# Optimization experiments

Hardware: AMD Instinct MI355X
Metric: run time of the kernel (lower is better)

Reference implementation:

```python
import jax, jax.numpy as jnp
import numpy as np

B, S, D = 4, 2048, 512
H, HD = 8, 64            # n_heads, head_dim = D // H
E, K, F = 8, 2, 1024     # n_experts, top_k, d_ff
EPS = 1e-6


def setup_inputs() -> dict:
    key = jax.random.key(0)
    ks = jax.random.split(key, 16)
    sd = 0.02
    return {
        "inputs": jax.random.normal(ks[0], (B, S, D), jnp.float32),
        "rms1_w": jnp.ones((D,), jnp.float32),
        "wq": jax.random.normal(ks[1], (D, H, HD), jnp.float32) * sd,
        "bq": jnp.zeros((H, HD), jnp.float32),
        "wk": jax.random.normal(ks[2], (D, H, HD), jnp.float32) * sd,
        "bk": jnp.zeros((H, HD), jnp.float32),
        "wv": jax.random.normal(ks[3], (D, H, HD), jnp.float32) * sd,
        "bv": jnp.zeros((H, HD), jnp.float32),
        "wo": jax.random.normal(ks[4], (H, HD, D), jnp.float32) * sd,
        "bo": jnp.zeros((D,), jnp.float32),
        "rms2_w": jnp.ones((D,), jnp.float32),
        "gate_w": jax.random.normal(ks[5], (D, E), jnp.float32) * sd,
        "ew1": jax.random.normal(ks[6], (E, D, F), jnp.float32) * sd,
        "eb1": jnp.zeros((E, F), jnp.float32),
        "ew2": jax.random.normal(ks[7], (E, F, D), jnp.float32) * sd,
        "eb2": jnp.zeros((E, D), jnp.float32),
    }


def _rmsnorm(x, w):
    return x * jax.lax.rsqrt(jnp.mean(x * x, axis=-1, keepdims=True) + EPS) * w


def _mha(x, wq, bq, wk, bk, wv, bv, wo, bo):
    q = jnp.einsum("bsd,dhe->bshe", x, wq) + bq
    k = jnp.einsum("bsd,dhe->bshe", x, wk) + bk
    v = jnp.einsum("bsd,dhe->bshe", x, wv) + bv
    scores = jnp.einsum("bqhe,bkhe->bhqk", q, k) / jnp.sqrt(jnp.float32(HD))
    attn = jax.nn.softmax(scores, axis=-1)
    ctx = jnp.einsum("bhqk,bkhe->bqhe", attn, v)
    return jnp.einsum("bqhe,hed->bqd", ctx, wo) + bo


def _moe(x, gate_w, ew1, eb1, ew2, eb2):
    T = B * S
    xt = x.reshape(T, D)
    probs = jax.nn.softmax(xt @ gate_w, axis=-1)          # [T, E]
    topv, topi = jax.lax.top_k(probs, K)                   # [T, K]
    topv = topv / jnp.sum(topv, axis=-1, keepdims=True)    # renormalize
    # dense combine weights [T, E]
    wmat = jnp.sum(jax.nn.one_hot(topi, E, dtype=xt.dtype) * topv[..., None], axis=1)
    h = jax.nn.relu(jnp.einsum("td,edf->tef", xt, ew1) + eb1)   # [T, E, F]
    y = jnp.einsum("tef,efd->ted", h, ew2) + eb2                # [T, E, D]
    out = jnp.einsum("te,ted->td", wmat, y)
    return out.reshape(B, S, D)


def reference(inputs, rms1_w, wq, bq, wk, bk, wv, bv, wo, bo, rms2_w, gate_w, ew1, eb1, ew2, eb2):
    x = _rmsnorm(inputs, rms1_w)
    x = _mha(x, wq, bq, wk, bk, wv, bv, wo, bo)
    x1 = x + inputs
    x = _rmsnorm(x1, rms2_w)
    x = _moe(x, gate_w, ew1, eb1, ew2, eb2)
    # dropout is identity at inference
    return x + x1
```

## Files before the change

kernel.cpp:

```cpp
#include <hip/hip_runtime.h>
#include <hip/hip_bf16.h>

typedef unsigned short u16;
typedef __attribute__((ext_vector_type(8))) short short8;
typedef __attribute__((ext_vector_type(4))) short bf16x4;
typedef __attribute__((ext_vector_type(4))) float f32x4;
typedef __attribute__((ext_vector_type(4))) int i32x4;
typedef __attribute__((ext_vector_type(2))) unsigned u32x2;

#define DEV __device__ __forceinline__

DEV float bf2f(u16 v){ unsigned u = ((unsigned)v)<<16; float f; __builtin_memcpy(&f,&u,4); return f; }
DEV u16 f2bf(float f){ unsigned u; __builtin_memcpy(&u,&f,4); u += 0x7fff + ((u>>16)&1); return (u16)(u>>16); }

DEV void gload16(const void* g, void* l){
  __builtin_amdgcn_global_load_lds((const __attribute__((address_space(1))) void*)g,
                                   (__attribute__((address_space(3))) void*)l, 16, 0, 0);
}

DEV unsigned packbf2(float a, float b){
  float2 f = {a, b};
  __hip_bfloat162 h = __float22bfloat162_rn(f);
  unsigned w; __builtin_memcpy(&w, &h, 4);
  return w;
}


__global__ __launch_bounds__(256) void k_tconv4(const float* __restrict__ s0, const float* __restrict__ s1,
    const float* __restrict__ s2, const float* __restrict__ s3, u16* __restrict__ dst){
  int z = blockIdx.z;
  const float* src = z==0 ? s0 : (z==1 ? s1 : (z==2 ? s2 : s3));
  dst += (size_t)z * 512 * 512;
  int r0 = blockIdx.y * 64, c0 = blockIdx.x * 64;
  __shared__ u16 tile[64][68];
  int tid = threadIdx.x;
  int rr = tid >> 4, cc = (tid & 15) * 4;
  #pragma unroll
  for (int it = 0; it < 4; ++it){
    int r = it*16 + rr;
    float4 v = *(const float4*)(src + (size_t)(r0 + r)*512 + c0 + cc);
    bf16x4 pk = { (short)f2bf(v.x), (short)f2bf(v.y), (short)f2bf(v.z), (short)f2bf(v.w) };
    *(bf16x4*)&tile[r][cc] = pk;
  }
  __syncthreads();
  #pragma unroll
  for (int it = 0; it < 4; ++it){
    int c = it*16 + rr;
    bf16x4 pk = { (short)tile[cc+0][c], (short)tile[cc+1][c],
                  (short)tile[cc+2][c], (short)tile[cc+3][c] };
    *(bf16x4*)(dst + (size_t)(c0 + c)*512 + r0 + cc) = pk;
  }
}

__global__ __launch_bounds__(256) void k_tconv(const float* __restrict__ src, u16* __restrict__ dst,
    int R, int C){
  src += (size_t)blockIdx.z * R * C;
  dst += (size_t)blockIdx.z * R * C;
  int r0 = blockIdx.y * 64, c0 = blockIdx.x * 64;
  __shared__ u16 tile[64][68];
  int tid = threadIdx.x;
  int rr = tid >> 4, cc = (tid & 15) * 4;
  #pragma unroll
  for (int it = 0; it < 4; ++it){
    int r = it*16 + rr;
    float4 v = *(const float4*)(src + (size_t)(r0 + r)*C + c0 + cc);
    bf16x4 pk = { (short)f2bf(v.x), (short)f2bf(v.y), (short)f2bf(v.z), (short)f2bf(v.w) };
    *(bf16x4*)&tile[r][cc] = pk;
  }
  __syncthreads();
  #pragma unroll
  for (int it = 0; it < 4; ++it){
    int c = it*16 + rr;
    bf16x4 pk = { (short)tile[cc+0][c], (short)tile[cc+1][c],
                  (short)tile[cc+2][c], (short)tile[cc+3][c] };
    *(bf16x4*)(dst + (size_t)(c0 + c)*R + r0 + cc) = pk;
  }
}

__global__ __launch_bounds__(256) void k_vtrans(const u16* __restrict__ src, u16* __restrict__ dst){
  int bh = blockIdx.y; int s0 = blockIdx.x*64;
  src += (size_t)bh*2048*64 + (size_t)s0*64;
  dst += (size_t)bh*64*2048 + s0;
  __shared__ unsigned tile[64*33];
  int tid = threadIdx.x;
  #pragma unroll
  for (int it = 0; it < 2; ++it){
    int c = tid + it*256;
    int r = c >> 3, c8 = c & 7;
    i32x4 v = *(const i32x4*)(src + (size_t)r*64 + c8*8);
    *(i32x4*)&tile[r*33 + c8*4] = v;
  }
  __syncthreads();
  #pragma unroll
  for (int it = 0; it < 2; ++it){
    int c = tid + it*256;
    int d = c >> 3, s8 = c & 7;
    union { i32x4 v; u16 us[8]; } o;
    #pragma unroll
    for (int j = 0; j < 8; ++j){
      unsigned w = tile[(s8*8+j)*33 + (d>>1)];
      o.us[j] = (d & 1) ? (u16)(w >> 16) : (u16)(w & 0xffff);
    }
    *(i32x4*)(dst + (size_t)d*2048 + s8*8) = o.v;
  }
}

__global__ __launch_bounds__(256) void k_rmsnorm(const float* __restrict__ x, const float* __restrict__ w,
    u16* __restrict__ ob){
  int t = blockIdx.x, tid = threadIdx.x;
  const float* xr = x + (size_t)t*512;
  float2 v = *(const float2*)(xr + tid*2);
  float ss = v.x*v.x + v.y*v.y;
  #pragma unroll
  for (int o=32; o>0; o>>=1) ss += __shfl_down(ss, o);
  __shared__ float sred[4];
  if ((tid&63)==0) sred[tid>>6] = ss;
  __syncthreads();
  float tot = sred[0]+sred[1]+sred[2]+sred[3];
  float inv = rsqrtf(tot*(1.f/512.f) + 1e-6f);
  float2 wv = *(const float2*)(w + tid*2);
  ob[(size_t)t*512 + tid*2]     = f2bf(v.x*inv*wv.x);
  ob[(size_t)t*512 + tid*2 + 1] = f2bf(v.y*inv*wv.y);
}

__global__ __launch_bounds__(256) void k_rmsgate(const float* __restrict__ x, const float* __restrict__ w,
    const float* __restrict__ gw, u16* __restrict__ ob, int* __restrict__ topi, float* __restrict__ topw){
  int t = blockIdx.x, tid = threadIdx.x;
  const float* xr = x + (size_t)t*512;
  float2 v = *(const float2*)(xr + tid*2);
  float ss = v.x*v.x + v.y*v.y;
  #pragma unroll
  for (int o=32; o>0; o>>=1) ss += __shfl_down(ss, o);
  __shared__ float sred[4];
  if ((tid&63)==0) sred[tid>>6] = ss;
  __syncthreads();
  float tot = sred[0]+sred[1]+sred[2]+sred[3];
  float inv = rsqrtf(tot*(1.f/512.f) + 1e-6f);
  float2 wv = *(const float2*)(w + tid*2);
  float y0 = v.x*inv*wv.x, y1 = v.y*inv*wv.y;
  ob[(size_t)t*512 + tid*2]     = f2bf(y0);
  ob[(size_t)t*512 + tid*2 + 1] = f2bf(y1);
  float acc[8];
  const float* g0 = gw + tid*16;
  #pragma unroll
  for (int e=0;e<8;e++) acc[e] = y0*g0[e] + y1*g0[8+e];
  #pragma unroll
  for (int dd=1; dd<64; dd<<=1)
    #pragma unroll
    for (int e=0;e<8;e++) acc[e] += __shfl_xor(acc[e], dd);
  __shared__ float gred[4][8];
  if ((tid&63)==0)
    #pragma unroll
    for (int e=0;e<8;e++) gred[tid>>6][e] = acc[e];
  __syncthreads();
  if (tid==0){
    float l[8];
    #pragma unroll
    for (int e=0;e<8;e++) l[e] = gred[0][e]+gred[1][e]+gred[2][e]+gred[3][e];
    int i0=0; float a0=l[0];
    #pragma unroll
    for (int e=1;e<8;e++) if (l[e]>a0){ a0=l[e]; i0=e; }
    int i1=-1; float a1=-1e30f;
    #pragma unroll
    for (int e=0;e<8;e++) if (e!=i0 && l[e]>a1){ a1=l[e]; i1=e; }
    float w1 = __expf(a1 - a0);
    float invs = 1.f / (1.f + w1);
    topi[t*2]=i0; topi[t*2+1]=i1;
    topw[t*2]=invs; topw[t*2+1]=w1*invs;
  }
}

__global__ __launch_bounds__(256) void k_count(const int* __restrict__ topi, int* __restrict__ counts){
  __shared__ int lcnt[8];
  if (threadIdx.x < 8) lcnt[threadIdx.x] = 0;
  __syncthreads();
  for (int i = blockIdx.x*256 + threadIdx.x; i < 16384; i += 256*64)
    atomicAdd(&lcnt[topi[i]], 1);
  __syncthreads();
  if (threadIdx.x < 8) atomicAdd(&counts[threadIdx.x], lcnt[threadIdx.x]);
}

template<int MODE>
__global__ __launch_bounds__(256) void k_gemm(const u16* __restrict__ A, const u16* __restrict__ Bt,
    int Nsize, int Ksize,
    const float* __restrict__ b0, const float* __restrict__ b1, const float* __restrict__ b2,
    const float* __restrict__ resid, float* __restrict__ outf,
    u16* __restrict__ o0, u16* __restrict__ o1, u16* __restrict__ o2,
    const int* __restrict__ ebase, const int* __restrict__ ecnt, const int* __restrict__ etok)
{
  int nNT = Nsize >> 7;
  int e=0, mt, nt, myBase=0, myCnt=0;
  if constexpr (MODE>=2){
    e = blockIdx.x & 7;
    int rr = blockIdx.x >> 3;
    mt = rr / nNT; nt = rr - mt*nNT;
    myCnt = ecnt[e]; myBase = ebase[e];
    if (mt*128 >= myCnt) return;
    Bt += (size_t)e * Nsize * Ksize;
  } else {
    int q = gridDim.x >> 3;
    int bid = blockIdx.x;
    int swb = (bid & 7)*q + (bid >> 3);
    mt = swb / nNT; nt = swb - mt*nNT;
  }
  __shared__ u16 As[2][128*32];
  __shared__ u16 Bs[2][128*32];
  int tid = threadIdx.x;
  int lane = tid & 63, wid = tid >> 6;
  int wr = (wid>>1)<<6, wc = (wid&1)<<6;
  int lrow = lane & 15, lk8 = (lane>>4)<<3;
  const u16* asrc[2]; const u16* bsrc[2];
  int ldoff[2];
  #pragma unroll
  for (int it=0; it<2; ++it){
    int c = it*256 + tid;
    int r = c >> 2, c4 = c & 3;
    int grow;
    if constexpr (MODE==2){
      int ml = mt*128 + r; if (ml >= myCnt) ml = myCnt-1;
      grow = etok[myBase + ml];
    } else if constexpr (MODE==3){
      int ml = mt*128 + r; if (ml >= myCnt) ml = myCnt-1;
      grow = myBase + ml;
    } else {
      grow = mt*128 + r;
    }
    asrc[it] = A + (size_t)grow*Ksize + c4*8;
    bsrc[it] = Bt + (size_t)(nt*128 + r)*Ksize + c4*8;
    ldoff[it] = (it*256 + wid*64)*8;
  }
  f32x4 acc[4][4] = {};
  int nK = Ksize >> 5;
  #pragma unroll
  for (int it=0; it<2; ++it){
    gload16(asrc[it], &As[0][ldoff[it]]);
    gload16(bsrc[it], &Bs[0][ldoff[it]]);
  }
  __syncthreads();
  for (int ks = 0; ks < nK; ++ks){
    int cur = ks & 1;
    if (ks+1 < nK){
      int k0 = (ks+1) << 5;
      #pragma unroll
      for (int it=0; it<2; ++it){
        gload16(asrc[it] + k0, &As[cur^1][ldoff[it]]);
        gload16(bsrc[it] + k0, &Bs[cur^1][ldoff[it]]);
      }
    }
    short8 a[4], b[4];
    #pragma unroll
    for (int i=0;i<4;i++) a[i] = *(const short8*)(&As[cur][(wr + i*16 + lrow)*32 + lk8]);
    #pragma unroll
    for (int j=0;j<4;j++) b[j] = *(const short8*)(&Bs[cur][(wc + j*16 + lrow)*32 + lk8]);
    #pragma unroll
    for (int i=0;i<4;i++)
      #pragma unroll
      for (int j=0;j<4;j++)
        acc[i][j] = __builtin_amdgcn_mfma_f32_16x16x32_bf16(a[i], b[j], acc[i][j], 0,0,0);
    __syncthreads();
  }
  #pragma unroll
  for (int i=0;i<4;i++){
    #pragma unroll
    for (int r=0;r<4;r++){
      int rowl = mt*128 + wr + i*16 + ((lane>>4)<<2) + r;
      #pragma unroll
      for (int j=0;j<4;j++){
        int col = nt*128 + wc + j*16 + lrow;
        float v = acc[i][j][r];
        if constexpr (MODE==0){
          int which = col >> 9; int hc = col & 511;
          const float* bias = which==0 ? b0 : (which==1 ? b1 : b2);
          v += bias[hc];
          if (which == 0) v *= 0.18033688011112042f;
          u16* dst = which==0 ? o0 : (which==1 ? o1 : o2);
          int bidx = rowl >> 11, s = rowl & 2047;
          int h = hc >> 6, hd = hc & 63;
          dst[((size_t)(bidx*8+h)*2048 + s)*64 + hd] = f2bf(v);
        } else if constexpr (MODE==1){
          v += b0[col] + resid[(size_t)rowl*512 + col];
          outf[(size_t)rowl*512 + col] = v;
        } else if constexpr (MODE==2){
          if (rowl < myCnt){
            v += b0[e*1024 + col];
            v = fmaxf(v, 0.f);
            o0[(size_t)(myBase+rowl)*1024 + col] = f2bf(v);
          }
        } else {
          if (rowl < myCnt){
            v += b0[e*512 + col];
            o0[(size_t)(myBase+rowl)*512 + col] = f2bf(v);
          }
        }
      }
    }
  }
}

__global__ __launch_bounds__(512) void k_attn(const u16* __restrict__ qb, const u16* __restrict__ kb,
    const u16* __restrict__ vtb, u16* __restrict__ ctx)
{
  int bh = blockIdx.x & 31;
  int qt = blockIdx.x >> 5;
  int b = bh >> 3, h = bh & 7;
  const size_t bho = (size_t)bh * (2048*64);
  int tid = threadIdx.x, lane = tid & 63, wid = tid >> 6;
  int lrow = lane & 15, g = lane >> 4;
  __shared__ u16 Ks[128*64];
  __shared__ u16 Vts[64*128];
  __shared__ u16 Ps[8][16*128];
  char* Ksb = (char*)Ks;
  char* Vsb = (char*)Vts;
  char* Psb = (char*)&Ps[wid][0];
  int q0 = qt*128 + wid*16;
  short8 qf[2];
  #pragma unroll
  for (int kf=0;kf<2;kf++)
    qf[kf] = *(const short8*)(qb + bho + (size_t)(q0 + lrow)*64 + kf*32 + g*8);
  f32x4 oacc[4] = {};
  float lpart = 0.f;
  const int swz = (lrow & 7) << 4;

  size_t ksrc[2], vsrc[2];
  int kdst[2], vdst[2];
  #pragma unroll
  for (int it=0; it<2; ++it){
    int c = tid + it*512;
    int kr = c >> 3, kc8 = c & 7;
    ksrc[it] = bho + (size_t)kr*64 + kc8*8;
    kdst[it] = kr*128 + ((kc8*16) ^ ((kr&7)<<4));
    int vr = c >> 4, vc16 = c & 15;
    vsrc[it] = bho + (size_t)vr*2048 + vc16*8;
    vdst[it] = vr*256 + ((vc16*16) ^ ((vr&7)<<4));
  }
  i32x4 kreg[2], vreg[2];
  #pragma unroll
  for (int it=0; it<2; ++it){
    kreg[it] = *(const i32x4*)(kb + ksrc[it]);
    vreg[it] = *(const i32x4*)(vtb + vsrc[it]);
  }
  #pragma unroll
  for (int it=0; it<2; ++it){
    *(i32x4*)(Ksb + kdst[it]) = kreg[it];
    *(i32x4*)(Vsb + vdst[it]) = vreg[it];
  }
  __syncthreads();

  for (int kt=0; kt<16; ++kt){
    if (kt < 15){
      int k0 = (kt+1)*128;
      #pragma unroll
      for (int it=0; it<2; ++it){
        kreg[it] = *(const i32x4*)(kb + ksrc[it] + (size_t)k0*64);
        vreg[it] = *(const i32x4*)(vtb + vsrc[it] + k0);
      }
    }
    __builtin_amdgcn_s_setprio(1);
    #pragma unroll
    for (int nf=0; nf<8; ++nf){
      short8 kf0 = *(const short8*)(Ksb + (nf*16+lrow)*128 + ((g*16) ^ swz));
      short8 kf1 = *(const short8*)(Ksb + (nf*16+lrow)*128 + ((64 + g*16) ^ swz));
      f32x4 s = {};
      s = __builtin_amdgcn_mfma_f32_16x16x32_bf16(kf0, qf[0], s, 0,0,0);
      s = __builtin_amdgcn_mfma_f32_16x16x32_bf16(kf1, qf[1], s, 0,0,0);
      float p0 = __builtin_amdgcn_exp2f(s[0]);
      float p1 = __builtin_amdgcn_exp2f(s[1]);
      float p2 = __builtin_amdgcn_exp2f(s[2]);
      float p3 = __builtin_amdgcn_exp2f(s[3]);
      lpart += (p0+p1)+(p2+p3);
      *(u32x2*)(Psb + lrow*256 + ((nf*32 + g*8) ^ swz)) = (u32x2){packbf2(p0,p1), packbf2(p2,p3)};
    }
    short8 pfr[4];
    #pragma unroll
    for (int kf=0;kf<4;kf++)
      pfr[kf] = *(const short8*)(Psb + lrow*256 + ((kf*64 + g*16) ^ swz));
    #pragma unroll
    for (int dn=0;dn<4;dn++){
      #pragma unroll
      for (int kf=0;kf<4;kf++){
        short8 vf = *(const short8*)(Vsb + (dn*16+lrow)*256 + ((kf*64 + g*16) ^ swz));
        oacc[dn] = __builtin_amdgcn_mfma_f32_16x16x32_bf16(pfr[kf], vf, oacc[dn], 0,0,0);
      }
    }
    __builtin_amdgcn_s_setprio(0);
    __syncthreads();
    if (kt < 15){
      #pragma unroll
      for (int it=0; it<2; ++it){
        *(i32x4*)(Ksb + kdst[it]) = kreg[it];
        *(i32x4*)(Vsb + vdst[it]) = vreg[it];
      }
      __syncthreads();
    }
  }
  float ls = lpart;
  ls += __shfl_xor(ls, 16);
  ls += __shfl_xor(ls, 32);
  float linv[4];
  #pragma unroll
  for (int r=0;r<4;r++)
    linv[r] = 1.0f / __shfl(ls, g*4 + r);
  #pragma unroll
  for (int r=0;r<4;r++){
    int qrow = q0 + g*4 + r;
    #pragma unroll
    for (int dn=0;dn<4;dn++)
      ctx[((size_t)(b*2048 + qrow))*512 + h*64 + dn*16 + lrow] = f2bf(oacc[dn][r] * linv[r]);
  }
}

__global__ void k_scan(const int* __restrict__ counts, int* __restrict__ base, int* __restrict__ cur){
  if (threadIdx.x==0 && blockIdx.x==0){
    int s=0;
    for (int e=0;e<8;e++){ base[e]=s; cur[e]=s; s+=counts[e]; }
  }
}

__global__ __launch_bounds__(256) void k_assign(const int* __restrict__ topi,
    int* __restrict__ cur, int* __restrict__ rowof, int* __restrict__ tokof)
{
  __shared__ int lcnt[8];
  __shared__ int gbase[8];
  int tid = threadIdx.x;
  if (tid < 8) lcnt[tid] = 0;
  __syncthreads();
  int t = blockIdx.x*256 + tid;
  int e0 = topi[t*2], e1 = topi[t*2+1];
  int r0 = atomicAdd(&lcnt[e0], 1);
  int r1 = atomicAdd(&lcnt[e1], 1);
  __syncthreads();
  if (tid < 8) gbase[tid] = atomicAdd(&cur[tid], lcnt[tid]);
  __syncthreads();
  int row0 = gbase[e0] + r0, row1 = gbase[e1] + r1;
  rowof[t*2]   = row0;  rowof[t*2+1] = row1;
  tokof[row0] = t;      tokof[row1] = t;
}

__global__ __launch_bounds__(256) void k_combine(const float* __restrict__ x1, const u16* __restrict__ y,
    const int* __restrict__ rowof, const float* __restrict__ topw, float* __restrict__ out)
{
  int idx = blockIdx.x*256 + threadIdx.x;
  int t = idx >> 7, dq = idx & 127;
  int r0 = rowof[t*2], r1 = rowof[t*2+1];
  float w0 = topw[t*2], w1 = topw[t*2+1];
  size_t o = (size_t)t*512 + dq*4;
  float4 x = *(const float4*)(x1 + o);
  bf16x4 y0 = *(const bf16x4*)(y + (size_t)r0*512 + dq*4);
  bf16x4 y1 = *(const bf16x4*)(y + (size_t)r1*512 + dq*4);
  float4 r;
  r.x = x.x + w0*bf2f((u16)y0[0]) + w1*bf2f((u16)y1[0]);
  r.y = x.y + w0*bf2f((u16)y0[1]) + w1*bf2f((u16)y1[1]);
  r.z = x.z + w0*bf2f((u16)y0[2]) + w1*bf2f((u16)y1[2]);
  r.w = x.w + w0*bf2f((u16)y0[3]) + w1*bf2f((u16)y1[3]);
  *(float4*)(out + o) = r;
}

extern "C" void kernel_launch(void* const* d_in, const int* in_sizes, int n_in,
                              void* d_out, int out_size, void* d_ws, size_t ws_size,
                              hipStream_t stream)
{
  const float* inputs = (const float*)d_in[0];
  const float* rms1_w = (const float*)d_in[1];
  const float* wq  = (const float*)d_in[2];
  const float* bq  = (const float*)d_in[3];
  const float* wk  = (const float*)d_in[4];
  const float* bk  = (const float*)d_in[5];
  const float* wv  = (const float*)d_in[6];
  const float* bv  = (const float*)d_in[7];
  const float* wo  = (const float*)d_in[8];
  const float* bo  = (const float*)d_in[9];
  const float* rms2_w = (const float*)d_in[10];
  const float* gate_w = (const float*)d_in[11];
  const float* ew1 = (const float*)d_in[12];
  const float* eb1 = (const float*)d_in[13];
  const float* ew2 = (const float*)d_in[14];
  const float* eb2 = (const float*)d_in[15];
  char* ws = (char*)d_ws;

  size_t off = 0;
  u16* WQKV = (u16*)(ws + off); off += 1536ull*512*2;
  u16* WOT  = (u16*)(ws + off); off += 512ull*512*2;
  u16* E1T  = (u16*)(ws + off); off += 8ull*1024*512*2;
  u16* E2T  = (u16*)(ws + off); off += 8ull*512*1024*2;
  u16* XN   = (u16*)(ws + off); u16* Hbuf = XN;      off += 8192ull*512*2;
  u16* Qb   = (u16*)(ws + off); off += 4ull*8*2048*64*2;
  u16* Kb   = (u16*)(ws + off); off += 4ull*8*2048*64*2;
  u16* Vb   = (u16*)(ws + off); off += 4ull*8*2048*64*2;
  u16* CTX  = (u16*)(ws + off); u16* Yb = CTX;       off += 8192ull*512*2;
  float* XN2F = (float*)(ws + off); u16* VbT = (u16*)XN2F; off += 8192ull*512*4;
  float* X1   = (float*)(ws + off); off += 8192ull*512*4;
  u16* XN2B   = (u16*)(ws + off); off += 8192ull*512*2;
  int*   TOPI = (int*)(ws + off); off += 16384*4;
  float* TOPW = (float*)(ws + off); off += 16384*4;
  int*  ROWOF = (int*)(ws + off); off += 16384*4;
  int*  TOKOF = (int*)(ws + off); off += 16384*4;
  int*  CNT   = (int*)(ws + off); off += 64;
  int*  BASE  = (int*)(ws + off); off += 64;
  int*  CUR   = (int*)(ws + off); off += 64;
  if (ws_size < off) return;
  (void)XN2F;

  k_tconv4<<<dim3(8,8,4),  256, 0, stream>>>(wq, wk, wv, wo, WQKV);
  k_tconv<<<dim3(16,8,8),  256, 0, stream>>>(ew1, E1T,  512, 1024);
  k_tconv<<<dim3(8,16,8),  256, 0, stream>>>(ew2, E2T, 1024,  512);

  k_rmsnorm<<<8192, 256, 0, stream>>>(inputs, rms1_w, XN);

  k_gemm<0><<<64*12, 256, 0, stream>>>(XN, WQKV, 1536, 512, bq, bk, bv,
      nullptr, nullptr, Qb, Kb, Vb, nullptr, nullptr, nullptr);

  k_vtrans<<<dim3(32,32), 256, 0, stream>>>(Vb, VbT);

  k_attn<<<512, 512, 0, stream>>>(Qb, Kb, VbT, CTX);

  k_gemm<1><<<64*4, 256, 0, stream>>>(CTX, WOT, 512, 512, bo, nullptr, nullptr,
      inputs, X1, nullptr, nullptr, nullptr, nullptr, nullptr, nullptr);

  k_rmsgate<<<8192, 256, 0, stream>>>(X1, rms2_w, gate_w, XN2B, TOPI, TOPW);

  hipMemsetAsync(CNT, 0, 192, stream);
  k_count<<<64, 256, 0, stream>>>(TOPI, CNT);
  k_scan<<<1, 64, 0, stream>>>(CNT, BASE, CUR);
  k_assign<<<32, 256, 0, stream>>>(TOPI, CUR, ROWOF, TOKOF);

  k_gemm<2><<<8*128*8, 256, 0, stream>>>(XN2B, E1T, 1024, 512, eb1, nullptr, nullptr,
      nullptr, nullptr, Hbuf, nullptr, nullptr, BASE, CNT, TOKOF);
  k_gemm<3><<<8*128*4, 256, 0, stream>>>(Hbuf, E2T, 512, 1024, eb2, nullptr, nullptr,
      nullptr, nullptr, Yb, nullptr, nullptr, BASE, CNT, TOKOF);

  k_combine<<<4096, 256, 0, stream>>>(X1, Yb, ROWOF, TOPW, (float*)d_out);
}
```

Before: 225.3 us.

## Enlarge attention blocks to 1024 threads and split P staging into halves

The attention kernel now uses 16 waves per block, each covering 256 query rows, and launches half as many blocks. Every K/V tile loaded into shared memory is therefore reused by twice as many query rows, and each thread loads one chunk instead of two. The per-wave P buffer is halved by handling the 128-key tile in two 64-key halves, keeping LDS usage the same despite the doubled wave count. The risks are only 256 blocks, which is about one per CU, so occupancy is coarse, plus the register cap that 1024-thread blocks impose and heavier barriers.

```diff
diff --git a/kernel.cpp b/kernel.cpp
--- a/kernel.cpp
+++ b/kernel.cpp
@@ -297,7 +297,7 @@
   }
 }
 
-__global__ __launch_bounds__(512) void k_attn(const u16* __restrict__ qb, const u16* __restrict__ kb,
+__global__ __launch_bounds__(1024) void k_attn(const u16* __restrict__ qb, const u16* __restrict__ kb,
     const u16* __restrict__ vtb, u16* __restrict__ ctx)
 {
   int bh = blockIdx.x & 31;
@@ -308,11 +308,11 @@
   int lrow = lane & 15, g = lane >> 4;
   __shared__ u16 Ks[128*64];
   __shared__ u16 Vts[64*128];
-  __shared__ u16 Ps[8][16*128];
+  __shared__ u16 Ps[16][16*64];
   char* Ksb = (char*)Ks;
   char* Vsb = (char*)Vts;
   char* Psb = (char*)&Ps[wid][0];
-  int q0 = qt*128 + wid*16;
+  int q0 = qt*256 + wid*16;
   short8 qf[2];
   #pragma unroll
   for (int kf=0;kf<2;kf++)
@@ -321,75 +321,62 @@
   float lpart = 0.f;
   const int swz = (lrow & 7) << 4;
 
-  size_t ksrc[2], vsrc[2];
-  int kdst[2], vdst[2];
-  #pragma unroll
-  for (int it=0; it<2; ++it){
-    int c = tid + it*512;
-    int kr = c >> 3, kc8 = c & 7;
-    ksrc[it] = bho + (size_t)kr*64 + kc8*8;
-    kdst[it] = kr*128 + ((kc8*16) ^ ((kr&7)<<4));
-    int vr = c >> 4, vc16 = c & 15;
-    vsrc[it] = bho + (size_t)vr*2048 + vc16*8;
-    vdst[it] = vr*256 + ((vc16*16) ^ ((vr&7)<<4));
-  }
-  i32x4 kreg[2], vreg[2];
-  #pragma unroll
-  for (int it=0; it<2; ++it){
-    kreg[it] = *(const i32x4*)(kb + ksrc[it]);
-    vreg[it] = *(const i32x4*)(vtb + vsrc[it]);
-  }
-  #pragma unroll
-  for (int it=0; it<2; ++it){
-    *(i32x4*)(Ksb + kdst[it]) = kreg[it];
-    *(i32x4*)(Vsb + vdst[it]) = vreg[it];
-  }
+  int c = tid;
+  int kr = c >> 3, kc8 = c & 7;
+  size_t ksrc = bho + (size_t)kr*64 + kc8*8;
+  int kdst = kr*128 + ((kc8*16) ^ ((kr&7)<<4));
+  int vr = c >> 4, vc16 = c & 15;
+  size_t vsrc = bho + (size_t)vr*2048 + vc16*8;
+  int vdst = vr*256 + ((vc16*16) ^ ((vr&7)<<4));
+
+  i32x4 kreg = *(const i32x4*)(kb + ksrc);
+  i32x4 vreg = *(const i32x4*)(vtb + vsrc);
+  *(i32x4*)(Ksb + kdst) = kreg;
+  *(i32x4*)(Vsb + vdst) = vreg;
   __syncthreads();
 
   for (int kt=0; kt<16; ++kt){
     if (kt < 15){
       int k0 = (kt+1)*128;
+      kreg = *(const i32x4*)(kb + ksrc + (size_t)k0*64);
+      vreg = *(const i32x4*)(vtb + vsrc + k0);
+    }
+    __builtin_amdgcn_s_setprio(1);
+    #pragma unroll
+    for (int hf=0; hf<2; ++hf){
       #pragma unroll
-      for (int it=0; it<2; ++it){
-        kreg[it] = *(const i32x4*)(kb + ksrc[it] + (size_t)k0*64);
-        vreg[it] = *(const i32x4*)(vtb + vsrc[it] + k0);
+      for (int nf=0; nf<4; ++nf){
+        int krow = hf*64 + nf*16 + lrow;
+        short8 kf0 = *(const short8*)(Ksb + krow*128 + ((g*16) ^ swz));
+        short8 kf1 = *(const short8*)(Ksb + krow*128 + ((64 + g*16) ^ swz));
+        f32x4 s = {};
+        s = __builtin_amdgcn_mfma_f32_16x16x32_bf16(kf0, qf[0], s, 0,0,0);
+        s = __builtin_amdgcn_mfma_f32_16x16x32_bf16(kf1, qf[1], s, 0,0,0);
+        float p0 = __builtin_amdgcn_exp2f(s[0]);
+        float p1 = __builtin_amdgcn_exp2f(s[1]);
+        float p2 = __builtin_amdgcn_exp2f(s[2]);
+        float p3 = __builtin_amdgcn_exp2f(s[3]);
+        lpart += (p0+p1)+(p2+p3);
+        *(u32x2*)(Psb + lrow*128 + ((nf*32 + g*8) ^ swz)) = (u32x2){packbf2(p0,p1), packbf2(p2,p3)};
       }
-    }
-    __builtin_amdgcn_s_setprio(1);
-    #pragma unroll
-    for (int nf=0; nf<8; ++nf){
-      short8 kf0 = *(const short8*)(Ksb + (nf*16+lrow)*128 + ((g*16) ^ swz));
-      short8 kf1 = *(const short8*)(Ksb + (nf*16+lrow)*128 + ((64 + g*16) ^ swz));
-      f32x4 s = {};
-      s = __builtin_amdgcn_mfma_f32_16x16x32_bf16(kf0, qf[0], s, 0,0,0);
-      s = __builtin_amdgcn_mfma_f32_16x16x32_bf16(kf1, qf[1], s, 0,0,0);
-      float p0 = __builtin_amdgcn_exp2f(s[0]);
-      float p1 = __builtin_amdgcn_exp2f(s[1]);
-      float p2 = __builtin_amdgcn_exp2f(s[2]);
-      float p3 = __builtin_amdgcn_exp2f(s[3]);
-      lpart += (p0+p1)+(p2+p3);
-      *(u32x2*)(Psb + lrow*256 + ((nf*32 + g*8) ^ swz)) = (u32x2){packbf2(p0,p1), packbf2(p2,p3)};
-    }
-    short8 pfr[4];
-    #pragma unroll
-    for (int kf=0;kf<4;kf++)
-      pfr[kf] = *(const short8*)(Psb + lrow*256 + ((kf*64 + g*16) ^ swz));
-    #pragma unroll
-    for (int dn=0;dn<4;dn++){
+      short8 pfr[2];
       #pragma unroll
-      for (int kf=0;kf<4;kf++){
-        short8 vf = *(const short8*)(Vsb + (dn*16+lrow)*256 + ((kf*64 + g*16) ^ swz));
-        oacc[dn] = __builtin_amdgcn_mfma_f32_16x16x32_bf16(pfr[kf], vf, oacc[dn], 0,0,0);
+      for (int kf=0;kf<2;kf++)
+        pfr[kf] = *(const short8*)(Psb + lrow*128 + ((kf*64 + g*16) ^ swz));
+      #pragma unroll
+      for (int dn=0;dn<4;dn++){
+        #pragma unroll
+        for (int kf=0;kf<2;kf++){
+          short8 vf = *(const short8*)(Vsb + (dn*16+lrow)*256 + ((hf*128 + kf*64 + g*16) ^ swz));
+          oacc[dn] = __builtin_amdgcn_mfma_f32_16x16x32_bf16(pfr[kf], vf, oacc[dn], 0,0,0);
+        }
       }
     }
     __builtin_amdgcn_s_setprio(0);
     __syncthreads();
     if (kt < 15){
-      #pragma unroll
-      for (int it=0; it<2; ++it){
-        *(i32x4*)(Ksb + kdst[it]) = kreg[it];
-        *(i32x4*)(Vsb + vdst[it]) = vreg[it];
-      }
+      *(i32x4*)(Ksb + kdst) = kreg;
+      *(i32x4*)(Vsb + vdst) = vreg;
       __syncthreads();
     }
   }
@@ -511,7 +498,7 @@
 
   k_vtrans<<<dim3(32,32), 256, 0, stream>>>(Vb, VbT);
 
-  k_attn<<<512, 512, 0, stream>>>(Qb, Kb, VbT, CTX);
+  k_attn<<<256, 1024, 0, stream>>>(Qb, Kb, VbT, CTX);
 
   k_gemm<1><<<64*4, 256, 0, stream>>>(CTX, WOT, 512, 512, bo, nullptr, nullptr,
       inputs, X1, nullptr, nullptr, nullptr, nullptr, nullptr, nullptr);
```

Result: no change. 223.5 us, median of 2 (-0.8%).
